# Optimization experiments

Hardware: AMD Instinct MI355X
Metric: run time of the kernel (lower is better)

## Reference

```python
import jax, jax.numpy as jnp
import numpy as np

SEQLEN = 64   # decoder loop length (forward scalar arg)
B = 32        # batch
S = 8192      # context_size (number of context vectors)
D = 256       # hidden_size == context_dim


def setup_inputs() -> dict:
    key = jax.random.key(0)
    k1, k2, k3, k4, k5 = jax.random.split(key, 5)
    hidden = jax.random.normal(k1, (1, B, D), dtype=jnp.float32)
    contextvects = jax.random.normal(k2, (B, D, S), dtype=jnp.float32)
    # nn.Linear(hidden_size=D, context_dim=D): W is [out=D, in=D], b is [D]
    W = jax.random.normal(k3, (D, D), dtype=jnp.float32) / np.sqrt(D).astype(np.float32)
    b = jax.random.normal(k4, (D,), dtype=jnp.float32) * 0.01
    # so no row is fully masked in practice
    padding_mask = jax.random.uniform(k5, (B, S, 1)) < 0.1
    return {"seqlen": SEQLEN, "hidden": hidden, "contextvects": contextvects,
            "W": W, "b": b, "padding_mask": padding_mask}


def reference(seqlen, hidden, contextvects, W, b, padding_mask):
    # context_proj = attn(contextvects.permute(0,2,1)) : [B, S, D]
    # (d = hidden_size input axis, e = context_dim output axis)
    context_proj = jnp.einsum('bds,ed->bse', contextvects, W) + b
    # attn_scores = context_proj @ hidden.permute(1,2,0) : [B, S, 1]
    scores = jnp.matmul(context_proj, jnp.transpose(hidden, (1, 2, 0)))
    scores = jnp.where(padding_mask, -jnp.inf, scores)
    attn = jax.nn.softmax(scores, axis=1)                 # [B, S, 1]
    ctx = jnp.matmul(contextvects, attn)[..., 0]          # [B, D]
    # the torch loop writes identical values for every i in range(seqlen)
    context = jnp.broadcast_to(ctx[None], (seqlen, B, D))
    attentions = jnp.broadcast_to(attn[..., 0][None], (seqlen, B, S))
    return context, attentions
```

## Files before the change

### kernel.cpp

```cpp
#include <hip/hip_runtime.h>
#include <math.h>

#define B_ 32
#define S_ 8192
#define D_ 256
#define TS 64
#define TPB 8
#define BPB (S_ / (TS * TPB))
#define CSHIFT 40.0f


__global__ __launch_bounds__(256) void k_wh(const float* __restrict__ W,
                                            const float* __restrict__ h,
                                            float* __restrict__ wh) {
  const int b = blockIdx.x;
  const int d = threadIdx.x;
  __shared__ float hs[D_];
  hs[d] = h[b * D_ + d];
  __syncthreads();
  float acc = 0.f;
#pragma unroll 8
  for (int e = 0; e < D_; ++e) acc = fmaf(W[e * D_ + d], hs[e], acc);
  wh[b * D_ + d] = acc;
}

__global__ __launch_bounds__(512, 4) void k_fused(const float* __restrict__ cv,
                                                  const float* __restrict__ wh,
                                                  const int* __restrict__ mask,
                                                  float* __restrict__ sc,
                                                  float* __restrict__ lpart,
                                                  float* __restrict__ opart) {
  __shared__ float scpart[2][2048];
  __shared__ float opred[8][512];

  const int b = blockIdx.y;
  const int blk = blockIdx.x;
  const int t = threadIdx.x;
  const int rq = t >> 4;
  const int cq = t & 15;
  const int mycol = t & 63;
  const int s_base = blk * (TS * TPB);
  const float* cvb = cv + (size_t)b * D_ * S_;

  float wh8[8];
#pragma unroll
  for (int it = 0; it < 8; ++it) wh8[it] = wh[b * D_ + rq + 32 * it];

  int mpack = 0;
#pragma unroll
  for (int tt = 0; tt < TPB; ++tt)
    if (mask[b * S_ + s_base + tt * TS + mycol] != 0) mpack |= 1 << tt;

  float o[8];
#pragma unroll
  for (int it = 0; it < 8; ++it) o[it] = 0.f;
  float lsum = 0.f;

#pragma unroll 1
  for (int tt = 0; tt < TPB; ++tt) {
    const int c0 = s_base + tt * TS;
    const int pb = tt & 1;

    float4 v[8];
#pragma unroll
    for (int it = 0; it < 8; ++it)
      v[it] = *reinterpret_cast<const float4*>(
          cvb + (size_t)(rq + 32 * it) * S_ + c0 + 4 * cq);

    float4 p; p.x = 0.f; p.y = 0.f; p.z = 0.f; p.w = 0.f;
#pragma unroll
    for (int it = 0; it < 8; ++it) {
      p.x = fmaf(v[it].x, wh8[it], p.x);
      p.y = fmaf(v[it].y, wh8[it], p.y);
      p.z = fmaf(v[it].z, wh8[it], p.z);
      p.w = fmaf(v[it].w, wh8[it], p.w);
    }
    *reinterpret_cast<float4*>(&scpart[pb][t * 4]) = p;
    __syncthreads();

    float a0 = 0.f, a1 = 0.f;
#pragma unroll
    for (int k = 0; k < 32; k += 2) {
      a0 += scpart[pb][k * 64 + mycol];
      a1 += scpart[pb][(k + 1) * 64 + mycol];
    }
    float sv = a0 + a1;
    if ((mpack >> tt) & 1) sv = -INFINITY;
    if (t < 64) sc[(size_t)b * S_ + c0 + t] = sv;

    const float e = __expf(sv - CSHIFT);
    lsum += e;

    const float p0 = __shfl(e, 4 * cq + 0, 64);
    const float p1 = __shfl(e, 4 * cq + 1, 64);
    const float p2 = __shfl(e, 4 * cq + 2, 64);
    const float p3 = __shfl(e, 4 * cq + 3, 64);
#pragma unroll
    for (int it = 0; it < 8; ++it)
      o[it] += v[it].x * p0 + v[it].y * p1 + v[it].z * p2 + v[it].w * p3;
  }

#pragma unroll
  for (int it = 0; it < 8; ++it) opred[it][t] = o[it];
  __syncthreads();
  if (t < 256) {
    float od = 0.f;
    const int k0 = 16 * (t & 31);
    const int itq = t >> 5;
#pragma unroll
    for (int q = 0; q < 16; ++q) od += opred[itq][k0 + q];
    opart[((size_t)b * BPB + blk) * D_ + t] = od;
  }

  if (t < 64) {
    float l = lsum;
#pragma unroll
    for (int off = 32; off > 0; off >>= 1) l += __shfl_xor(l, off, 64);
    if (t == 0) lpart[(size_t)b * BPB + blk] = l;
  }
}

__global__ __launch_bounds__(256) void k_out(const float* __restrict__ lpart,
                                             const float* __restrict__ opart,
                                             const float* __restrict__ sc,
                                             float* __restrict__ out,
                                             int seqlen) {
  const int nAttn = seqlen * B_;
  const int id = blockIdx.x;
  const int t = threadIdx.x;
  __shared__ float sI;

  if (id < nAttn) {
    const int i = id >> 5;
    const int b = id & 31;
    if (t < 64) {
      float lv = (t < BPB) ? lpart[(size_t)b * BPB + t] : 0.f;
#pragma unroll
      for (int off = 32; off > 0; off >>= 1) lv += __shfl_xor(lv, off, 64);
      if (t == 0) sI = 1.0f / lv;
    }
    __syncthreads();
    const float invL = sI;
    float4* dst = reinterpret_cast<float4*>(
        out + (size_t)seqlen * B_ * D_ + ((size_t)i * B_ + b) * S_);
    const float4* src = reinterpret_cast<const float4*>(sc + (size_t)b * S_);
#pragma unroll
    for (int j = 0; j < S_ / 4 / 256; ++j) {
      const int q = j * 256 + t;
      const float4 v = src[q];
      float4 r;
      r.x = __expf(v.x - CSHIFT) * invL;
      r.y = __expf(v.y - CSHIFT) * invL;
      r.z = __expf(v.z - CSHIFT) * invL;
      r.w = __expf(v.w - CSHIFT) * invL;
      dst[q] = r;
    }
  } else {
    const int j = id - nAttn;
    const int i = j >> 3;
    const int b = (j & 7) * 4 + (t >> 6);
    const int lane = t & 63;
    float lv = (lane < BPB) ? lpart[(size_t)b * BPB + lane] : 0.f;
#pragma unroll
    for (int off = 32; off > 0; off >>= 1) lv += __shfl_xor(lv, off, 64);
    const float invL = 1.0f / lv;

    float4 acc; acc.x = 0.f; acc.y = 0.f; acc.z = 0.f; acc.w = 0.f;
#pragma unroll
    for (int ti = 0; ti < BPB; ++ti) {
      const float4 op = *reinterpret_cast<const float4*>(
          opart + ((size_t)b * BPB + ti) * D_ + 4 * lane);
      acc.x += op.x; acc.y += op.y; acc.z += op.z; acc.w += op.w;
    }
    acc.x *= invL; acc.y *= invL; acc.z *= invL; acc.w *= invL;
    *reinterpret_cast<float4*>(out + ((size_t)i * B_ + b) * D_ + 4 * lane) = acc;
  }
}

extern "C" void kernel_launch(void* const* d_in, const int* in_sizes, int n_in,
                              void* d_out, int out_size, void* d_ws, size_t ws_size,
                              hipStream_t stream) {
  const float* hidden = (const float*)d_in[1];
  const float* cv = (const float*)d_in[2];
  const float* W = (const float*)d_in[3];
  const int* mask = (const int*)d_in[5];

  float* ws = (float*)d_ws;
  float* wh = ws;
  float* sc = ws + 16384;
  float* lpart = ws + 278528;
  float* opart = ws + 280576;

  const int seqlen = out_size / (B_ * D_ + B_ * S_);

  k_wh<<<B_, D_, 0, stream>>>(W, hidden, wh);
  k_fused<<<dim3(BPB, B_), 512, 0, stream>>>(cv, wh, mask, sc, lpart, opart);
  k_out<<<seqlen * B_ + seqlen * 8, 256, 0, stream>>>(lpart, opart, sc,
                                                      (float*)d_out, seqlen);
}
```

Baseline: 86.11 us.

## Fuse W·h projection into main kernel and use nontemporal output stores

Removes the separate k_wh launch. Each fused block now recomputes the 256x256 W^T·h product for its batch into shared memory before streaming the context tile, which saves one kernel launch and the global round-trip for wh. The cost is redundant work: every one of the BPB blocks per batch reads the full 256 KB W matrix and does 64K FMAs. The output writes in k_out also switch to nontemporal stores, so the large broadcast attention output does not pollute the cache.

```diff
diff --git a/kernel.cpp b/kernel.cpp
--- a/kernel.cpp
+++ b/kernel.cpp
@@ -9,29 +9,20 @@
 #define BPB (S_ / (TS * TPB))
 #define CSHIFT 40.0f
 
-
-__global__ __launch_bounds__(256) void k_wh(const float* __restrict__ W,
-                                            const float* __restrict__ h,
-                                            float* __restrict__ wh) {
-  const int b = blockIdx.x;
-  const int d = threadIdx.x;
-  __shared__ float hs[D_];
-  hs[d] = h[b * D_ + d];
-  __syncthreads();
-  float acc = 0.f;
-#pragma unroll 8
-  for (int e = 0; e < D_; ++e) acc = fmaf(W[e * D_ + d], hs[e], acc);
-  wh[b * D_ + d] = acc;
-}
+typedef float vf4 __attribute__((ext_vector_type(4)));
+
 
 __global__ __launch_bounds__(512, 4) void k_fused(const float* __restrict__ cv,
-                                                  const float* __restrict__ wh,
+                                                  const float* __restrict__ W,
+                                                  const float* __restrict__ h,
                                                   const int* __restrict__ mask,
                                                   float* __restrict__ sc,
                                                   float* __restrict__ lpart,
                                                   float* __restrict__ opart) {
   __shared__ float scpart[2][2048];
   __shared__ float opred[8][512];
+  __shared__ float whs[D_];
+  __shared__ float hh[D_];
 
   const int b = blockIdx.y;
   const int blk = blockIdx.x;
@@ -42,9 +33,19 @@
   const int s_base = blk * (TS * TPB);
   const float* cvb = cv + (size_t)b * D_ * S_;
 
+  if (t < D_) hh[t] = h[b * D_ + t];
+  __syncthreads();
+  if (t < D_) {
+    float acc = 0.f;
+#pragma unroll 8
+    for (int e = 0; e < D_; ++e) acc = fmaf(W[e * D_ + t], hh[e], acc);
+    whs[t] = acc;
+  }
+  __syncthreads();
+
   float wh8[8];
 #pragma unroll
-  for (int it = 0; it < 8; ++it) wh8[it] = wh[b * D_ + rq + 32 * it];
+  for (int it = 0; it < 8; ++it) wh8[it] = whs[rq + 32 * it];
 
   int mpack = 0;
 #pragma unroll
@@ -141,19 +142,19 @@
     }
     __syncthreads();
     const float invL = sI;
-    float4* dst = reinterpret_cast<float4*>(
+    vf4* dst = reinterpret_cast<vf4*>(
         out + (size_t)seqlen * B_ * D_ + ((size_t)i * B_ + b) * S_);
     const float4* src = reinterpret_cast<const float4*>(sc + (size_t)b * S_);
 #pragma unroll
     for (int j = 0; j < S_ / 4 / 256; ++j) {
       const int q = j * 256 + t;
       const float4 v = src[q];
-      float4 r;
+      vf4 r;
       r.x = __expf(v.x - CSHIFT) * invL;
       r.y = __expf(v.y - CSHIFT) * invL;
       r.z = __expf(v.z - CSHIFT) * invL;
       r.w = __expf(v.w - CSHIFT) * invL;
-      dst[q] = r;
+      __builtin_nontemporal_store(r, &dst[q]);
     }
   } else {
     const int j = id - nAttn;
@@ -165,7 +166,7 @@
     for (int off = 32; off > 0; off >>= 1) lv += __shfl_xor(lv, off, 64);
     const float invL = 1.0f / lv;
 
-    float4 acc; acc.x = 0.f; acc.y = 0.f; acc.z = 0.f; acc.w = 0.f;
+    vf4 acc = (vf4)0.f;
 #pragma unroll
     for (int ti = 0; ti < BPB; ++ti) {
       const float4 op = *reinterpret_cast<const float4*>(
@@ -173,7 +174,8 @@
       acc.x += op.x; acc.y += op.y; acc.z += op.z; acc.w += op.w;
     }
     acc.x *= invL; acc.y *= invL; acc.z *= invL; acc.w *= invL;
-    *reinterpret_cast<float4*>(out + ((size_t)i * B_ + b) * D_ + 4 * lane) = acc;
+    vf4* cdst = reinterpret_cast<vf4*>(out + ((size_t)i * B_ + b) * D_ + 4 * lane);
+    __builtin_nontemporal_store(acc, cdst);
   }
 }
 
@@ -186,15 +188,13 @@
   const int* mask = (const int*)d_in[5];
 
   float* ws = (float*)d_ws;
-  float* wh = ws;
   float* sc = ws + 16384;
   float* lpart = ws + 278528;
   float* opart = ws + 280576;
 
   const int seqlen = out_size / (B_ * D_ + B_ * S_);
 
-  k_wh<<<B_, D_, 0, stream>>>(W, hidden, wh);
-  k_fused<<<dim3(BPB, B_), 512, 0, stream>>>(cv, wh, mask, sc, lpart, opart);
+  k_fused<<<dim3(BPB, B_), 512, 0, stream>>>(cv, W, hidden, mask, sc, lpart, opart);
   k_out<<<seqlen * B_ + seqlen * 8, 256, 0, stream>>>(lpart, opart, sc,
                                                       (float*)d_out, seqlen);
 }
```

Result: faster. 69.80 us (-18.9%).
